# Performance work log

Hardware: AMD Instinct MI355X
Metric: run time of the kernel (lower is better)

The kernel has to match this reference:

```python
import jax, jax.numpy as jnp
import numpy as np

B, T, S, D = 8, 128, 512, 128  # batch, decoder steps, encoder len, output_dim==input_dim


def setup_inputs() -> dict:
    key = jax.random.key(0)
    ks = jax.random.split(key, 24)
    g = lambda i, shape: jax.random.normal(ks[i], shape, dtype=jnp.float32) * 0.05
    inp = {
        "x": g(0, (B, T, D)),
        "H": g(1, (B, S, D)),
        "init_states": jnp.zeros((2, B, D), jnp.float32),
        "Wa": g(2, (D, D)), "Ua": g(3, (D, D)), "v": g(4, (D,)),
        "Wi": g(5, (D, D)), "Ui": g(6, (D, D)), "Ci": g(7, (D, D)), "bi": jnp.zeros((D,), jnp.float32),
        "Wf": g(8, (D, D)), "Uf": g(9, (D, D)), "Cf": g(10, (D, D)), "bf": jnp.ones((D,), jnp.float32),
        "Wc": g(11, (D, D)), "Uc": g(12, (D, D)), "Cc": g(13, (D, D)), "bc": jnp.zeros((D,), jnp.float32),
        "Wo": g(14, (D, D)), "Uo": g(15, (D, D)), "Co": g(16, (D, D)), "bo": jnp.zeros((D,), jnp.float32),
    }
    return inp


def _forward(x, H, init_states, Wa, Ua, v, Wi, Ui, Ci, bi, Wf, Uf, Cf, bf,
             Wc, Uc, Cc, bc, Wo, Uo, Co, bo):
    # A = H @ Ua is loop-invariant in the original step(); hoist it (same math).
    HU = jnp.einsum('bsd,de->bse', H, Ua)  # [B,S,D]

    def step(carry, x_t):
        h_prev, c_prev = carry  # each [B,D]
        # Bahdanau attention over the full encoder sequence
        q = h_prev @ Wa                                        # [B,D]
        score = jnp.einsum('bsd,d->bs', jnp.tanh(HU + q[:, None, :]), v)  # [B,S]
        a = jax.nn.softmax(score, axis=-1)                     # [B,S]
        context = jnp.einsum('bsd,bs->bd', H, a)               # [B,D]
        # 4-gate LSTM update
        i_g = jax.nn.sigmoid(x_t @ Wi + h_prev @ Ui + context @ Ci + bi)
        f_g = jax.nn.sigmoid(x_t @ Wf + h_prev @ Uf + context @ Cf + bf)
        g_w = jnp.tanh(x_t @ Wc + h_prev @ Uc + context @ Cc + bc)
        c_t = f_g * c_prev + i_g * g_w
        o_g = jax.nn.sigmoid(x_t @ Wo + h_prev @ Uo + context @ Co + bo)
        h_t = o_g * jnp.tanh(c_t)
        return (h_t, c_t), h_t

    h0, c0 = init_states[0], init_states[1]
    x_tm = jnp.transpose(x, (1, 0, 2))  # time-major [T,B,D]
    _, hs = jax.lax.scan(step, (h0, c0), x_tm)  # hs: [T,B,D]
    return jnp.transpose(hs, (1, 0, 2))  # [B,T,D] hidden states (original returns [0] of stacked [h,c])


def reference(x, H, init_states, Wa, Ua, v, Wi, Ui, Ci, bi, Wf, Uf, Cf, bf,
              Wc, Uc, Cc, bc, Wo, Uo, Co, bo):
    return _forward(x, H, init_states, Wa, Ua, v, Wi, Ui, Ci, bi, Wf, Uf, Cf, bf,
                    Wc, Uc, Cc, bc, Wo, Uo, Co, bo)
```

## Files before the change

kernel.cpp:

```cpp
#include <hip/hip_runtime.h>

#define DEV __device__ __forceinline__

constexpr int nB = 8, nT = 128, nS = 512, nD = 128;
constexpr int J   = 4;
constexpr int SL  = 128;
constexpr int NTH = 512;

constexpr int S1_CNT = nB * J * 130;
constexpr int S2_OFF = S1_CNT;
constexpr int S2_CNT = nB * J * 32;
constexpr int XW_F   = (S1_CNT + S2_CNT) * 2;

DEV float tanh_small(float x) {
    float x2 = x * x;
    float p = fmaf(x2, 0.133333333f, -0.333333333f);
    return fmaf(x * x2, p, x);
}
DEV float fast_tanh(float x) {
    x = fminf(4.0f, fmaxf(-4.0f, x));
    float x2 = x * x;
    float num = fmaf(fmaf(x2 + 378.0f, x2, 17325.0f), x2, 135135.0f);
    float den = fmaf(fmaf(fmaf(x2, 28.0f, 3150.0f), x2, 62370.0f), x2, 135135.0f);
    return x * num * __builtin_amdgcn_rcpf(den);
}
DEV float fast_sig(float x) { return fmaf(fast_tanh(0.5f * x), 0.5f, 0.5f); }

typedef unsigned long long u64;
DEV u64  pk(float v, unsigned tag) { return ((u64)tag << 32) | (u64)__float_as_uint(v); }
DEV void st64(u64* p, u64 v) { __hip_atomic_store(p, v, __ATOMIC_RELAXED, __HIP_MEMORY_SCOPE_AGENT); }
DEV u64  ld64(const u64* p)  { return __hip_atomic_load(p, __ATOMIC_RELAXED, __HIP_MEMORY_SCOPE_AGENT); }
DEV float poll64(const u64* p, unsigned want) {
    for (;;) {
        u64 q = ld64(p);
        if ((unsigned)(q >> 32) == want) return __uint_as_float((unsigned)q);
        __builtin_amdgcn_s_sleep(1);
    }
}

__global__ void init_kernel(float* __restrict__ ws) {
    u64* p = (u64*)ws;
    for (int i = threadIdx.x; i < S1_CNT + S2_CNT; i += 1024)
        __hip_atomic_store(p + i, 0ull, __ATOMIC_RELAXED, __HIP_MEMORY_SCOPE_AGENT);
}

__global__ __launch_bounds__(NTH, 1) void attn_lstm_kernel(
    const float* __restrict__ x,  const float* __restrict__ H,
    const float* __restrict__ init_states, const float* __restrict__ Wa,
    const float* __restrict__ Ua, const float* __restrict__ v,
    const float* __restrict__ Wi, const float* __restrict__ Ui,
    const float* __restrict__ Ci, const float* __restrict__ bi,
    const float* __restrict__ Wf, const float* __restrict__ Uf,
    const float* __restrict__ Cf, const float* __restrict__ bf,
    const float* __restrict__ Wc, const float* __restrict__ Uc,
    const float* __restrict__ Cc, const float* __restrict__ bc,
    const float* __restrict__ Wo, const float* __restrict__ Uo,
    const float* __restrict__ Co, const float* __restrict__ bo,
    float* __restrict__ out, float* __restrict__ ws)
{
    const int tid = threadIdx.x;
    const int b = blockIdx.x & 7;
    const int j = blockIdx.x >> 3;

    u64*   S1   = (u64*)ws;
    u64*   S2   = (u64*)ws + S2_OFF;
    float* wsXW = ws + XW_F;

    __shared__ __align__(16) float Hs[SL * nD];
    __shared__ __align__(16) float q_l[nD];
    __shared__ __align__(16) float ctx_l[nD];
    __shared__ __align__(16) float h_l[nD];
    __shared__ __align__(16) float e_l[SL];
    __shared__ float sc_l[SL];
    __shared__ float pre_l[nD];
    __shared__ float pNx[3 * nD];
    __shared__ float mS_l[8];

    const int hi = tid >> 2, lo = tid & 3;
    const int g = hi >> 5, dd = hi & 31, gcol = 32 * j + dd;

    const float* Ug = (g == 0) ? Ui : (g == 1) ? Uf : (g == 2) ? Uc : Uo;
    const float* Cg = (g == 0) ? Ci : (g == 1) ? Cf : (g == 2) ? Cc : Co;
    const float* Bg = (g == 0) ? bi : (g == 1) ? bf : (g == 2) ? bc : bo;

    {
        for (int k = tid; k < 16384; k += NTH) {
            int gg = k >> 12, r = (k >> 5) & 127, i = k & 31;
            const float* Wm = (gg == 0) ? Wi : (gg == 1) ? Wf : (gg == 2) ? Wc : Wo;
            Hs[k] = Wm[r * nD + 32 * j + i];
        }
    }
    __syncthreads();

    {
        float acc[32];
        #pragma unroll
        for (int i = 0; i < 32; ++i) acc[i] = 0.0f;
        const float* xrow = x + ((size_t)b * nT + hi) * nD;
        for (int r = 0; r < nD; ++r) {
            float xr = xrow[r];
            const float* wrow = &Hs[lo * 4096 + r * 32];
            #pragma unroll
            for (int i = 0; i < 32; ++i) acc[i] = fmaf(xr, wrow[i], acc[i]);
        }
        float* dst = wsXW + ((size_t)(b * J + j) * nT + hi) * nD + lo * 32;
        #pragma unroll
        for (int k = 0; k < 8; ++k)
            ((float4*)dst)[k] = make_float4(acc[4*k], acc[4*k+1], acc[4*k+2], acc[4*k+3]);
    }
    __syncthreads();

    for (int k = tid; k < 16384; k += NTH) Hs[k] = Ua[k];
    __syncthreads();

    float HU_r[32];
    {
        #pragma unroll
        for (int i = 0; i < 32; ++i) HU_r[i] = 0.0f;
        const float* hrow = H + ((size_t)b * nS + (size_t)SL * j + hi) * nD;
        for (int r = 0; r < nD; ++r) {
            float hr = hrow[r];
            const float* uar = &Hs[r * nD + lo * 32];
            #pragma unroll
            for (int i = 0; i < 32; ++i) HU_r[i] = fmaf(hr, uar[i], HU_r[i]);
        }
    }
    __syncthreads();

    {
        const float* hrow = H + ((size_t)b * nS + (size_t)SL * j + hi) * nD + lo * 32;
        int c = hi >> 4, w = hi & 15;
        #pragma unroll
        for (int k = 0; k < 8; ++k) {
            float4 hv = ((const float4*)hrow)[k];
            int d0 = lo * 32 + 4 * k;
            Hs[(d0+0) * nD + ((c ^ ((d0+0) & 7)) * 16) + w] = hv.x;
            Hs[(d0+1) * nD + ((c ^ ((d0+1) & 7)) * 16) + w] = hv.y;
            Hs[(d0+2) * nD + ((c ^ ((d0+2) & 7)) * 16) + w] = hv.z;
            Hs[(d0+3) * nD + ((c ^ ((d0+3) & 7)) * 16) + w] = hv.w;
        }
    }

    float wa_r[32], u_r[32], c_r2[32], v_r[32];
    #pragma unroll
    for (int i = 0; i < 32; ++i) {
        wa_r[i] = Wa[(lo * 32 + i) * nD + hi];
        u_r[i]  = Ug[(lo * 32 + i) * nD + gcol];
        c_r2[i] = Cg[(lo * 32 + i) * nD + gcol];
        v_r[i]  = v[lo * 32 + i];
    }
    const float bval = Bg[gcol];
    float c_reg = (tid < 32) ? init_states[nB * nD + b * nD + 32 * j + tid] : 0.0f;

    if (tid < nD) h_l[tid] = init_states[b * nD + tid];
    __syncthreads();

    u64* myN = S1 + (size_t)(b * J + j) * 130;
    u64* myH = S2 + (size_t)(b * J + j) * 32;

    for (int t = 0; t < nT; ++t) {
        const unsigned tg = (unsigned)(t + 1);

        float xwv = 0.0f;
        if (lo == 0) xwv = wsXW[((size_t)(b * J + j) * nT + t) * nD + hi];

        float qa = 0.0f, uasum = 0.0f;
        #pragma unroll
        for (int i = 0; i < 32; ++i) {
            float hv = h_l[lo * 32 + i];
            qa    = fmaf(hv, wa_r[i], qa);
            uasum = fmaf(hv, u_r[i],  uasum);
        }
        qa += __shfl_xor(qa, 1);  qa += __shfl_xor(qa, 2);
        uasum += __shfl_xor(uasum, 1);  uasum += __shfl_xor(uasum, 2);
        if (lo == 0) q_l[hi] = qa;
        __syncthreads();

        float sa = 0.0f;
        #pragma unroll
        for (int k = 0; k < 8; ++k) {
            float4 qq = *(const float4*)&q_l[lo * 32 + 4 * k];
            sa = fmaf(v_r[4*k+0], tanh_small(HU_r[4*k+0] + qq.x), sa);
            sa = fmaf(v_r[4*k+1], tanh_small(HU_r[4*k+1] + qq.y), sa);
            sa = fmaf(v_r[4*k+2], tanh_small(HU_r[4*k+2] + qq.z), sa);
            sa = fmaf(v_r[4*k+3], tanh_small(HU_r[4*k+3] + qq.w), sa);
        }
        sa += __shfl_xor(sa, 1);  sa += __shfl_xor(sa, 2);
        if (lo == 0) sc_l[hi] = sa;
        __syncthreads();

        float m, se;
        {
            int lane = tid & 63;
            float s0 = sc_l[lane], s1 = sc_l[64 + lane];
            m = fmaxf(s0, s1);
            #pragma unroll
            for (int o = 1; o < 64; o <<= 1) m = fmaxf(m, __shfl_xor(m, o));
            float e0 = __expf(s0 - m), e1 = __expf(s1 - m);
            se = e0 + e1;
            #pragma unroll
            for (int o = 1; o < 64; o <<= 1) se += __shfl_xor(se, o);
            if (tid < 64) { e_l[tid] = e0; e_l[64 + tid] = e1; }
        }
        __syncthreads();

        float na = 0.0f;
        #pragma unroll
        for (int cc = 0; cc < 2; ++cc) {
            int c = 2 * lo + cc;
            int pc = c ^ (hi & 7);
            const float4* hp = (const float4*)&Hs[hi * nD + pc * 16];
            const float4* ep = (const float4*)&e_l[c * 16];
            #pragma unroll
            for (int k2 = 0; k2 < 4; ++k2) {
                float4 hh = hp[k2]; float4 ee = ep[k2];
                na = fmaf(ee.x, hh.x, na); na = fmaf(ee.y, hh.y, na);
                na = fmaf(ee.z, hh.z, na); na = fmaf(ee.w, hh.w, na);
            }
        }
        na += __shfl_xor(na, 1);  na += __shfl_xor(na, 2);

        if (lo == 0) st64(myN + hi, pk(na, tg));
        if (tid == 0) st64(myN + 128, pk(m, tg));
        if (tid == 1) st64(myN + 129, pk(se, tg));
        if (tid < 384) {
            int pi = tid >> 7, d2 = tid & 127;
            int jj = pi + (pi >= j);
            pNx[pi * nD + d2] = poll64(S1 + (size_t)(b * J + jj) * 130 + d2, tg);
        }
        if (tid >= 384 && tid < 390) {
            int k = tid - 384, pi = k >> 1, wh = k & 1;
            int jj = pi + (pi >= j);
            mS_l[pi * 2 + wh] = poll64(S1 + (size_t)(b * J + jj) * 130 + 128 + wh, tg);
        }
        __syncthreads();

        if (lo == 0) {
            float mm = m;
            #pragma unroll
            for (int p2 = 0; p2 < 3; ++p2) mm = fmaxf(mm, mS_l[p2 * 2]);
            float w0 = __expf(m - mm);
            float ssum = se * w0, nsum = na * w0;
            #pragma unroll
            for (int p2 = 0; p2 < 3; ++p2) {
                float wp = __expf(mS_l[p2 * 2] - mm);
                ssum = fmaf(mS_l[p2 * 2 + 1], wp, ssum);
                nsum = fmaf(pNx[p2 * nD + hi], wp, nsum);
            }
            ctx_l[hi] = nsum * __builtin_amdgcn_rcpf(ssum);
        }
        __syncthreads();

        float ca = 0.0f;
        #pragma unroll
        for (int i = 0; i < 32; ++i) ca = fmaf(ctx_l[lo * 32 + i], c_r2[i], ca);
        ca += __shfl_xor(ca, 1);  ca += __shfl_xor(ca, 2);
        if (lo == 0) pre_l[hi] = uasum + ca + xwv + bval;
        __syncthreads();

        if (tid < 32) {
            float p_i = pre_l[tid], p_f = pre_l[32 + tid];
            float p_c = pre_l[64 + tid], p_o = pre_l[96 + tid];
            float ig = fast_sig(p_i), fg = fast_sig(p_f);
            float gg = fast_tanh(p_c), og = fast_sig(p_o);
            c_reg = fmaf(fg, c_reg, ig * gg);
            float hn = og * fast_tanh(c_reg);
            st64(myH + tid, pk(hn, tg));
            h_l[32 * j + tid] = hn;
            out[((size_t)b * nT + t) * nD + 32 * j + tid] = hn;
        }
        if (tid >= 32 && tid < 128) {
            int k = tid - 32, pi = k >> 5, dd2 = k & 31;
            int jj = pi + (pi >= j);
            h_l[32 * jj + dd2] = poll64(S2 + (size_t)(b * J + jj) * 32 + dd2, tg);
        }
        __syncthreads();
    }
}

extern "C" void kernel_launch(void* const* d_in, const int* in_sizes, int n_in,
                              void* d_out, int out_size, void* d_ws, size_t ws_size,
                              hipStream_t stream) {
    const float* x  = (const float*)d_in[0];
    const float* H  = (const float*)d_in[1];
    const float* is = (const float*)d_in[2];
    const float* Wa = (const float*)d_in[3];
    const float* Ua = (const float*)d_in[4];
    const float* v  = (const float*)d_in[5];
    const float* Wi = (const float*)d_in[6];
    const float* Ui = (const float*)d_in[7];
    const float* Ci = (const float*)d_in[8];
    const float* bi = (const float*)d_in[9];
    const float* Wf = (const float*)d_in[10];
    const float* Uf = (const float*)d_in[11];
    const float* Cf = (const float*)d_in[12];
    const float* bf = (const float*)d_in[13];
    const float* Wc = (const float*)d_in[14];
    const float* Uc = (const float*)d_in[15];
    const float* Cc = (const float*)d_in[16];
    const float* bc = (const float*)d_in[17];
    const float* Wo = (const float*)d_in[18];
    const float* Uo = (const float*)d_in[19];
    const float* Co = (const float*)d_in[20];
    const float* bo = (const float*)d_in[21];
    float* out = (float*)d_out;
    float* ws  = (float*)d_ws;

    hipLaunchKernelGGL(init_kernel, dim3(1), dim3(1024), 0, stream, ws);
    hipLaunchKernelGGL(attn_lstm_kernel, dim3(nB * J), dim3(NTH), 0, stream,
                       x, H, is, Wa, Ua, v,
                       Wi, Ui, Ci, bi, Wf, Uf, Cf, bf,
                       Wc, Uc, Cc, bc, Wo, Uo, Co, bo,
                       out, ws);
}
```

Baseline: 805.1 us.

## Interleave two batches per block to hide cross-block sync latency

```diff
diff --git a/kernel.cpp b/kernel.cpp
--- a/kernel.cpp
+++ b/kernel.cpp
@@ -1,6 +1,7 @@
 #include <hip/hip_runtime.h>
 
 #define DEV __device__ __forceinline__
+typedef unsigned long long u64;
 
 constexpr int nB = 8, nT = 128, nS = 512, nD = 128;
 constexpr int J   = 4;
@@ -26,25 +27,146 @@
 }
 DEV float fast_sig(float x) { return fmaf(fast_tanh(0.5f * x), 0.5f, 0.5f); }
 
-typedef unsigned long long u64;
-DEV u64  pk(float v, unsigned tag) { return ((u64)tag << 32) | (u64)__float_as_uint(v); }
+DEV u64  pk(float v, unsigned t) { return ((u64)t << 32) | (u64)__float_as_uint(v); }
 DEV void st64(u64* p, u64 v) { __hip_atomic_store(p, v, __ATOMIC_RELAXED, __HIP_MEMORY_SCOPE_AGENT); }
 DEV u64  ld64(const u64* p)  { return __hip_atomic_load(p, __ATOMIC_RELAXED, __HIP_MEMORY_SCOPE_AGENT); }
 DEV float poll64(const u64* p, unsigned want) {
-    for (;;) {
-        u64 q = ld64(p);
-        if ((unsigned)(q >> 32) == want) return __uint_as_float((unsigned)q);
-        __builtin_amdgcn_s_sleep(1);
-    }
-}
-
-__global__ void init_kernel(float* __restrict__ ws) {
-    u64* p = (u64*)ws;
-    for (int i = threadIdx.x; i < S1_CNT + S2_CNT; i += 1024)
-        __hip_atomic_store(p + i, 0ull, __ATOMIC_RELAXED, __HIP_MEMORY_SCOPE_AGENT);
-}
-
-__global__ __launch_bounds__(NTH, 1) void attn_lstm_kernel(
+    u64 q = ld64(p);
+    while ((unsigned)(q >> 32) != want) q = ld64(p);
+    return __uint_as_float((unsigned)q);
+}
+DEV int swz(int d) { return ((((d >> 2) ^ (d >> 5)) << 2) | (d & 3)); }
+
+DEV void first_half(int tid, unsigned tg,
+    const float (&HU)[32], const float (&wa_r)[32], const float (&u_r)[32],
+    const float* __restrict__ h_l, const float* __restrict__ v_l,
+    const float* __restrict__ Ht,
+    float* __restrict__ q_l, float* __restrict__ sc_l, float* __restrict__ e_l,
+    u64* myN, float& uasum, float& na, float& m, float& se)
+{
+    const int hi = tid >> 2, lo = tid & 3;
+    float qa = 0.0f; uasum = 0.0f;
+    #pragma unroll
+    for (int k = 0; k < 8; ++k) {
+        float4 hv = *(const float4*)&h_l[(lo * 8 + (k ^ lo)) << 2];
+        qa = fmaf(hv.x, wa_r[4*k+0], qa); qa = fmaf(hv.y, wa_r[4*k+1], qa);
+        qa = fmaf(hv.z, wa_r[4*k+2], qa); qa = fmaf(hv.w, wa_r[4*k+3], qa);
+        uasum = fmaf(hv.x, u_r[4*k+0], uasum); uasum = fmaf(hv.y, u_r[4*k+1], uasum);
+        uasum = fmaf(hv.z, u_r[4*k+2], uasum); uasum = fmaf(hv.w, u_r[4*k+3], uasum);
+    }
+    qa += __shfl_xor(qa, 1); qa += __shfl_xor(qa, 2);
+    uasum += __shfl_xor(uasum, 1); uasum += __shfl_xor(uasum, 2);
+    if (lo == 0) q_l[swz(hi)] = qa;
+    __syncthreads();
+    float sa = 0.0f;
+    #pragma unroll
+    for (int k = 0; k < 8; ++k) {
+        float4 qq = *(const float4*)&q_l[(lo * 8 + (k ^ lo)) << 2];
+        float4 vv = *(const float4*)&v_l[lo * 32 + 4 * k];
+        sa = fmaf(vv.x, tanh_small(HU[4*k+0] + qq.x), sa);
+        sa = fmaf(vv.y, tanh_small(HU[4*k+1] + qq.y), sa);
+        sa = fmaf(vv.z, tanh_small(HU[4*k+2] + qq.z), sa);
+        sa = fmaf(vv.w, tanh_small(HU[4*k+3] + qq.w), sa);
+    }
+    sa += __shfl_xor(sa, 1); sa += __shfl_xor(sa, 2);
+    if (lo == 0) sc_l[hi] = sa;
+    __syncthreads();
+    {
+        int lane = tid & 63;
+        float s0 = sc_l[lane], s1 = sc_l[64 + lane];
+        m = fmaxf(s0, s1);
+        #pragma unroll
+        for (int o = 1; o < 64; o <<= 1) m = fmaxf(m, __shfl_xor(m, o));
+        float e0 = __expf(s0 - m), e1 = __expf(s1 - m);
+        se = e0 + e1;
+        #pragma unroll
+        for (int o = 1; o < 64; o <<= 1) se += __shfl_xor(se, o);
+        if (tid < 64) { e_l[tid] = e0; e_l[64 + tid] = e1; }
+    }
+    __syncthreads();
+    const int dm = (tid & 15) | ((tid >> 6) << 4);
+    const int le = (tid >> 4) & 3;
+    na = 0.0f;
+    #pragma unroll
+    for (int i = 0; i < 8; ++i) {
+        int phys = ((le * 8 + i) + dm) & 31;
+        float4 hh = *(const float4*)&Ht[dm * nD + phys * 4];
+        float4 ee = *(const float4*)&e_l[le * 32 + 4 * i];
+        na = fmaf(ee.x, hh.x, na); na = fmaf(ee.y, hh.y, na);
+        na = fmaf(ee.z, hh.z, na); na = fmaf(ee.w, hh.w, na);
+    }
+    na += __shfl_xor(na, 16); na += __shfl_xor(na, 32);
+    if ((tid & 48) == 0) st64(myN + dm, pk(na, tg));
+    if (tid == 0) st64(myN + 128, pk(m, tg));
+    if (tid == 1) st64(myN + 129, pk(se, tg));
+}
+
+DEV void second_half(int tid, int j, unsigned tg, const float (&c_r2)[32],
+    float na, float m, float se, float uasum, float xwv, float bval,
+    u64* __restrict__ S1, int bbJ,
+    float* __restrict__ pNx, float* __restrict__ mS_l,
+    float* __restrict__ ctx_l, float* __restrict__ pre_l,
+    float* __restrict__ h_l, u64* myH, float& c_reg, float* __restrict__ outp)
+{
+    if (tid < 384) {
+        int pi = tid >> 7, d2 = tid & 127, jj = pi + (pi >= j);
+        pNx[pi * nD + d2] = poll64(S1 + (size_t)(bbJ + jj) * 130 + d2, tg);
+    }
+    if (tid >= 384 && tid < 390) {
+        int k = tid - 384, pi = k >> 1, wh = k & 1, jj = pi + (pi >= j);
+        mS_l[2 * pi + wh] = poll64(S1 + (size_t)(bbJ + jj) * 130 + 128 + wh, tg);
+    }
+    __syncthreads();
+    const int dm = (tid & 15) | ((tid >> 6) << 4);
+    if ((tid & 48) == 0) {
+        float mm = m;
+        #pragma unroll
+        for (int p2 = 0; p2 < 3; ++p2) mm = fmaxf(mm, mS_l[2 * p2]);
+        float w0 = __expf(m - mm);
+        float ssum = se * w0, nsum = na * w0;
+        #pragma unroll
+        for (int p2 = 0; p2 < 3; ++p2) {
+            float wp = __expf(mS_l[2 * p2] - mm);
+            ssum = fmaf(mS_l[2 * p2 + 1], wp, ssum);
+            nsum = fmaf(pNx[p2 * nD + dm], wp, nsum);
+        }
+        ctx_l[swz(dm)] = nsum * __builtin_amdgcn_rcpf(ssum);
+    }
+    __syncthreads();
+    const int hi = tid >> 2, lo = tid & 3;
+    float ca = 0.0f;
+    #pragma unroll
+    for (int k = 0; k < 8; ++k) {
+        float4 cv = *(const float4*)&ctx_l[(lo * 8 + (k ^ lo)) << 2];
+        ca = fmaf(cv.x, c_r2[4*k+0], ca); ca = fmaf(cv.y, c_r2[4*k+1], ca);
+        ca = fmaf(cv.z, c_r2[4*k+2], ca); ca = fmaf(cv.w, c_r2[4*k+3], ca);
+    }
+    ca += __shfl_xor(ca, 1); ca += __shfl_xor(ca, 2);
+    if (lo == 0) pre_l[hi] = uasum + ca + xwv + bval;
+    __syncthreads();
+    if (tid < 32) {
+        float pI = pre_l[tid], pF = pre_l[32 + tid];
+        float pC = pre_l[64 + tid], pO = pre_l[96 + tid];
+        float ig = fast_sig(pI), fg = fast_sig(pF);
+        float gg = fast_tanh(pC), og = fast_sig(pO);
+        c_reg = fmaf(fg, c_reg, ig * gg);
+        float hn = og * fast_tanh(c_reg);
+        st64(myH + tid, pk(hn, tg));
+        h_l[swz(32 * j + tid)] = hn;
+        outp[32 * j + tid] = hn;
+    }
+}
+
+DEV void poll_h(int tid, int j, unsigned wtag, u64* __restrict__ S2v, int bbJ,
+                float* __restrict__ h_l)
+{
+    if (tid < 96) {
+        int pi = tid >> 5, dd = tid & 31, jj = pi + (pi >= j);
+        h_l[swz(32 * jj + dd)] = poll64(S2v + (size_t)(bbJ + jj) * 32 + dd, wtag);
+    }
+}
+
+__global__ __launch_bounds__(NTH, 2) void attn_lstm_kernel(
     const float* __restrict__ x,  const float* __restrict__ H,
     const float* __restrict__ init_states, const float* __restrict__ Wa,
     const float* __restrict__ Ua, const float* __restrict__ v,
@@ -59,222 +181,133 @@
     float* __restrict__ out, float* __restrict__ ws)
 {
     const int tid = threadIdx.x;
-    const int b = blockIdx.x & 7;
-    const int j = blockIdx.x >> 3;
+    const int p = blockIdx.x & 3, j = blockIdx.x >> 2;
+    const int b0 = 2 * p, b1 = 2 * p + 1;
 
     u64*   S1   = (u64*)ws;
-    u64*   S2   = (u64*)ws + S2_OFF;
+    u64*   S2v  = (u64*)ws + S2_OFF;
     float* wsXW = ws + XW_F;
 
-    __shared__ __align__(16) float Hs[SL * nD];
-    __shared__ __align__(16) float q_l[nD];
-    __shared__ __align__(16) float ctx_l[nD];
-    __shared__ __align__(16) float h_l[nD];
-    __shared__ __align__(16) float e_l[SL];
-    __shared__ float sc_l[SL];
-    __shared__ float pre_l[nD];
+    __shared__ __align__(16) float Ht0[SL * nD];
+    __shared__ __align__(16) float Ht1[SL * nD];
+    __shared__ __align__(16) float h_l0[nD], h_l1[nD];
+    __shared__ __align__(16) float q_l[nD], ctx_l[nD], pre_l[nD], v_l[nD];
+    __shared__ __align__(16) float sc_l[SL], e_l[SL];
     __shared__ float pNx[3 * nD];
     __shared__ float mS_l[8];
 
     const int hi = tid >> 2, lo = tid & 3;
-    const int g = hi >> 5, dd = hi & 31, gcol = 32 * j + dd;
-
+    const int g = hi >> 5, gcol = 32 * j + (hi & 31);
     const float* Ug = (g == 0) ? Ui : (g == 1) ? Uf : (g == 2) ? Uc : Uo;
     const float* Cg = (g == 0) ? Ci : (g == 1) ? Cf : (g == 2) ? Cc : Co;
     const float* Bg = (g == 0) ? bi : (g == 1) ? bf : (g == 2) ? bc : bo;
 
-    {
-        for (int k = tid; k < 16384; k += NTH) {
-            int gg = k >> 12, r = (k >> 5) & 127, i = k & 31;
-            const float* Wm = (gg == 0) ? Wi : (gg == 1) ? Wf : (gg == 2) ? Wc : Wo;
-            Hs[k] = Wm[r * nD + 32 * j + i];
-        }
-    }
-    __syncthreads();
-
-    {
+    for (int k = tid; k < 16384; k += NTH) {
+        int gg = k >> 12, r = (k >> 5) & 127, i = k & 31;
+        const float* Wm = (gg == 0) ? Wi : (gg == 1) ? Wf : (gg == 2) ? Wc : Wo;
+        Ht0[k] = Wm[r * nD + 32 * j + i];
+    }
+    __syncthreads();
+    for (int bb = 0; bb < 2; ++bb) {
+        const int bsel = (bb == 0) ? b0 : b1;
         float acc[32];
         #pragma unroll
         for (int i = 0; i < 32; ++i) acc[i] = 0.0f;
-        const float* xrow = x + ((size_t)b * nT + hi) * nD;
+        const float* xrow = x + ((size_t)bsel * nT + hi) * nD;
         for (int r = 0; r < nD; ++r) {
             float xr = xrow[r];
-            const float* wrow = &Hs[lo * 4096 + r * 32];
+            const float* wrow = &Ht0[lo * 4096 + r * 32];
             #pragma unroll
             for (int i = 0; i < 32; ++i) acc[i] = fmaf(xr, wrow[i], acc[i]);
         }
-        float* dst = wsXW + ((size_t)(b * J + j) * nT + hi) * nD + lo * 32;
-        #pragma unroll
-        for (int k = 0; k < 8; ++k)
-            ((float4*)dst)[k] = make_float4(acc[4*k], acc[4*k+1], acc[4*k+2], acc[4*k+3]);
-    }
-    __syncthreads();
-
-    for (int k = tid; k < 16384; k += NTH) Hs[k] = Ua[k];
-    __syncthreads();
-
-    float HU_r[32];
+        float* dst = wsXW + ((size_t)(bsel * J + j) * nT + hi) * nD + lo * 32;
+        #pragma unroll
+        for (int k2 = 0; k2 < 8; ++k2)
+            ((float4*)dst)[k2] = make_float4(acc[4*k2], acc[4*k2+1], acc[4*k2+2], acc[4*k2+3]);
+    }
+    __syncthreads();
+    for (int k = tid; k < 16384; k += NTH) Ht0[k] = Ua[k];
+    __syncthreads();
+    float HU0[32], HU1[32];
     {
         #pragma unroll
-        for (int i = 0; i < 32; ++i) HU_r[i] = 0.0f;
-        const float* hrow = H + ((size_t)b * nS + (size_t)SL * j + hi) * nD;
+        for (int i = 0; i < 32; ++i) { HU0[i] = 0.0f; HU1[i] = 0.0f; }
+        const float* hr0 = H + ((size_t)b0 * nS + (size_t)SL * j + hi) * nD;
+        const float* hr1 = H + ((size_t)b1 * nS + (size_t)SL * j + hi) * nD;
         for (int r = 0; r < nD; ++r) {
-            float hr = hrow[r];
-            const float* uar = &Hs[r * nD + lo * 32];
+            float a0 = hr0[r], a1 = hr1[r];
+            const float* uar = &Ht0[r * nD + lo * 32];
             #pragma unroll
-            for (int i = 0; i < 32; ++i) HU_r[i] = fmaf(hr, uar[i], HU_r[i]);
-        }
-    }
-    __syncthreads();
-
-    {
-        const float* hrow = H + ((size_t)b * nS + (size_t)SL * j + hi) * nD + lo * 32;
-        int c = hi >> 4, w = hi & 15;
-        #pragma unroll
-        for (int k = 0; k < 8; ++k) {
-            float4 hv = ((const float4*)hrow)[k];
-            int d0 = lo * 32 + 4 * k;
-            Hs[(d0+0) * nD + ((c ^ ((d0+0) & 7)) * 16) + w] = hv.x;
-            Hs[(d0+1) * nD + ((c ^ ((d0+1) & 7)) * 16) + w] = hv.y;
-            Hs[(d0+2) * nD + ((c ^ ((d0+2) & 7)) * 16) + w] = hv.z;
-            Hs[(d0+3) * nD + ((c ^ ((d0+3) & 7)) * 16) + w] = hv.w;
-        }
-    }
-
-    float wa_r[32], u_r[32], c_r2[32], v_r[32];
+            for (int i = 0; i < 32; ++i) {
+                float u = uar[i];
+                HU0[i] = fmaf(a0, u, HU0[i]);
+                HU1[i] = fmaf(a1, u, HU1[i]);
+            }
+        }
+    }
+    __syncthreads();
+    for (int bb = 0; bb < 2; ++bb) {
+        float* Ht = (bb == 0) ? Ht0 : Ht1;
+        const float* hrow = H + ((size_t)((bb == 0) ? b0 : b1) * nS + (size_t)SL * j + hi) * nD + lo * 32;
+        const int c = hi >> 2, w = hi & 3;
+        #pragma unroll
+        for (int k2 = 0; k2 < 8; ++k2) {
+            float4 hv = ((const float4*)hrow)[k2];
+            int d0 = lo * 32 + 4 * k2;
+            Ht[(d0+0) * nD + ((c + (d0+0)) & 31) * 4 + w] = hv.x;
+            Ht[(d0+1) * nD + ((c + (d0+1)) & 31) * 4 + w] = hv.y;
+            Ht[(d0+2) * nD + ((c + (d0+2)) & 31) * 4 + w] = hv.z;
+            Ht[(d0+3) * nD + ((c + (d0+3)) & 31) * 4 + w] = hv.w;
+        }
+    }
+    if (tid < nD) v_l[tid] = v[tid];
+
+    float wa_r[32], u_r[32], c_r2[32];
     #pragma unroll
     for (int i = 0; i < 32; ++i) {
         wa_r[i] = Wa[(lo * 32 + i) * nD + hi];
         u_r[i]  = Ug[(lo * 32 + i) * nD + gcol];
         c_r2[i] = Cg[(lo * 32 + i) * nD + gcol];
-        v_r[i]  = v[lo * 32 + i];
     }
     const float bval = Bg[gcol];
-    float c_reg = (tid < 32) ? init_states[nB * nD + b * nD + 32 * j + tid] : 0.0f;
-
-    if (tid < nD) h_l[tid] = init_states[b * nD + tid];
-    __syncthreads();
-
-    u64* myN = S1 + (size_t)(b * J + j) * 130;
-    u64* myH = S2 + (size_t)(b * J + j) * 32;
-
+    float c0 = 0.0f, c1 = 0.0f;
+    if (tid < 32) {
+        c0 = init_states[nB * nD + b0 * nD + 32 * j + tid];
+        c1 = init_states[nB * nD + b1 * nD + 32 * j + tid];
+    }
+    if (tid < nD) {
+        h_l0[swz(tid)] = init_states[b0 * nD + tid];
+        h_l1[swz(tid)] = init_states[b1 * nD + tid];
+    }
+    __syncthreads();
+
+    u64* myN0 = S1 + (size_t)(b0 * J + j) * 130;
+    u64* myN1 = S1 + (size_t)(b1 * J + j) * 130;
+    u64* myH0 = S2v + (size_t)(b0 * J + j) * 32;
+    u64* myH1 = S2v + (size_t)(b1 * J + j) * 32;
+
+    float uas0, na0, m0, se0, uas1, na1, m1, se1;
     for (int t = 0; t < nT; ++t) {
         const unsigned tg = (unsigned)(t + 1);
-
-        float xwv = 0.0f;
-        if (lo == 0) xwv = wsXW[((size_t)(b * J + j) * nT + t) * nD + hi];
-
-        float qa = 0.0f, uasum = 0.0f;
-        #pragma unroll
-        for (int i = 0; i < 32; ++i) {
-            float hv = h_l[lo * 32 + i];
-            qa    = fmaf(hv, wa_r[i], qa);
-            uasum = fmaf(hv, u_r[i],  uasum);
-        }
-        qa += __shfl_xor(qa, 1);  qa += __shfl_xor(qa, 2);
-        uasum += __shfl_xor(uasum, 1);  uasum += __shfl_xor(uasum, 2);
-        if (lo == 0) q_l[hi] = qa;
+        float xwv0 = 0.0f, xwv1 = 0.0f;
+        if (lo == 0) {
+            xwv0 = wsXW[((size_t)(b0 * J + j) * nT + t) * nD + hi];
+            xwv1 = wsXW[((size_t)(b1 * J + j) * nT + t) * nD + hi];
+        }
+        if (t) poll_h(tid, j, (unsigned)t, S2v, b0 * J, h_l0);
         __syncthreads();
-
-        float sa = 0.0f;
-        #pragma unroll
-        for (int k = 0; k < 8; ++k) {
-            float4 qq = *(const float4*)&q_l[lo * 32 + 4 * k];
-            sa = fmaf(v_r[4*k+0], tanh_small(HU_r[4*k+0] + qq.x), sa);
-            sa = fmaf(v_r[4*k+1], tanh_small(HU_r[4*k+1] + qq.y), sa);
-            sa = fmaf(v_r[4*k+2], tanh_small(HU_r[4*k+2] + qq.z), sa);
-            sa = fmaf(v_r[4*k+3], tanh_small(HU_r[4*k+3] + qq.w), sa);
-        }
-        sa += __shfl_xor(sa, 1);  sa += __shfl_xor(sa, 2);
-        if (lo == 0) sc_l[hi] = sa;
+        first_half(tid, tg, HU0, wa_r, u_r, h_l0, v_l, Ht0,
+                   q_l, sc_l, e_l, myN0, uas0, na0, m0, se0);
+        if (t) poll_h(tid, j, (unsigned)t, S2v, b1 * J, h_l1);
         __syncthreads();
-
-        float m, se;
-        {
-            int lane = tid & 63;
-            float s0 = sc_l[lane], s1 = sc_l[64 + lane];
-            m = fmaxf(s0, s1);
-            #pragma unroll
-            for (int o = 1; o < 64; o <<= 1) m = fmaxf(m, __shfl_xor(m, o));
-            float e0 = __expf(s0 - m), e1 = __expf(s1 - m);
-            se = e0 + e1;
-            #pragma unroll
-            for (int o = 1; o < 64; o <<= 1) se += __shfl_xor(se, o);
-            if (tid < 64) { e_l[tid] = e0; e_l[64 + tid] = e1; }
-        }
-        __syncthreads();
-
-        float na = 0.0f;
-        #pragma unroll
-        for (int cc = 0; cc < 2; ++cc) {
-            int c = 2 * lo + cc;
-            int pc = c ^ (hi & 7);
-            const float4* hp = (const float4*)&Hs[hi * nD + pc * 16];
-            const float4* ep = (const float4*)&e_l[c * 16];
-            #pragma unroll
-            for (int k2 = 0; k2 < 4; ++k2) {
-                float4 hh = hp[k2]; float4 ee = ep[k2];
-                na = fmaf(ee.x, hh.x, na); na = fmaf(ee.y, hh.y, na);
-                na = fmaf(ee.z, hh.z, na); na = fmaf(ee.w, hh.w, na);
-            }
-        }
-        na += __shfl_xor(na, 1);  na += __shfl_xor(na, 2);
-
-        if (lo == 0) st64(myN + hi, pk(na, tg));
-        if (tid == 0) st64(myN + 128, pk(m, tg));
-        if (tid == 1) st64(myN + 129, pk(se, tg));
-        if (tid < 384) {
-            int pi = tid >> 7, d2 = tid & 127;
-            int jj = pi + (pi >= j);
-            pNx[pi * nD + d2] = poll64(S1 + (size_t)(b * J + jj) * 130 + d2, tg);
-        }
-        if (tid >= 384 && tid < 390) {
-            int k = tid - 384, pi = k >> 1, wh = k & 1;
-            int jj = pi + (pi >= j);
-            mS_l[pi * 2 + wh] = poll64(S1 + (size_t)(b * J + jj) * 130 + 128 + wh, tg);
-        }
-        __syncthreads();
-
-        if (lo == 0) {
-            float mm = m;
-            #pragma unroll
-            for (int p2 = 0; p2 < 3; ++p2) mm = fmaxf(mm, mS_l[p2 * 2]);
-            float w0 = __expf(m - mm);
-            float ssum = se * w0, nsum = na * w0;
-            #pragma unroll
-            for (int p2 = 0; p2 < 3; ++p2) {
-                float wp = __expf(mS_l[p2 * 2] - mm);
-                ssum = fmaf(mS_l[p2 * 2 + 1], wp, ssum);
-                nsum = fmaf(pNx[p2 * nD + hi], wp, nsum);
-            }
-            ctx_l[hi] = nsum * __builtin_amdgcn_rcpf(ssum);
-        }
-        __syncthreads();
-
-        float ca = 0.0f;
-        #pragma unroll
-        for (int i = 0; i < 32; ++i) ca = fmaf(ctx_l[lo * 32 + i], c_r2[i], ca);
-        ca += __shfl_xor(ca, 1);  ca += __shfl_xor(ca, 2);
-        if (lo == 0) pre_l[hi] = uasum + ca + xwv + bval;
-        __syncthreads();
-
-        if (tid < 32) {
-            float p_i = pre_l[tid], p_f = pre_l[32 + tid];
-            float p_c = pre_l[64 + tid], p_o = pre_l[96 + tid];
-            float ig = fast_sig(p_i), fg = fast_sig(p_f);
-            float gg = fast_tanh(p_c), og = fast_sig(p_o);
-            c_reg = fmaf(fg, c_reg, ig * gg);
-            float hn = og * fast_tanh(c_reg);
-            st64(myH + tid, pk(hn, tg));
-            h_l[32 * j + tid] = hn;
-            out[((size_t)b * nT + t) * nD + 32 * j + tid] = hn;
-        }
-        if (tid >= 32 && tid < 128) {
-            int k = tid - 32, pi = k >> 5, dd2 = k & 31;
-            int jj = pi + (pi >= j);
-            h_l[32 * jj + dd2] = poll64(S2 + (size_t)(b * J + jj) * 32 + dd2, tg);
-        }
-        __syncthreads();
+        first_half(tid, tg, HU1, wa_r, u_r, h_l1, v_l, Ht1,
+                   q_l, sc_l, e_l, myN1, uas1, na1, m1, se1);
+        second_half(tid, j, tg, c_r2, na0, m0, se0, uas0, xwv0, bval,
+                    S1, b0 * J, pNx, mS_l, ctx_l, pre_l, h_l0, myH0, c0,
+                    out + ((size_t)b0 * nT + t) * nD);
+        second_half(tid, j, tg, c_r2, na1, m1, se1, uas1, xwv1, bval,
+                    S1, b1 * J, pNx, mS_l, ctx_l, pre_l, h_l1, myH1, c1,
+                    out + ((size_t)b1 * nT + t) * nD);
     }
 }
 
@@ -306,8 +339,7 @@
     float* out = (float*)d_out;
     float* ws  = (float*)d_ws;
 
-    hipLaunchKernelGGL(init_kernel, dim3(1), dim3(1024), 0, stream, ws);
-    hipLaunchKernelGGL(attn_lstm_kernel, dim3(nB * J), dim3(NTH), 0, stream,
+    hipLaunchKernelGGL(attn_lstm_kernel, dim3(nB * J / 2), dim3(NTH), 0, stream,
                        x, H, is, Wa, Ua, v,
                        Wi, Ui, Ci, bi, Wf, Uf, Cf, bf,
                        Wc, Uc, Cc, bc, Wo, Uo, Co, bo,
```

Measured after the change: 1.604 ms. 99.3% more time.
